# Kernel tuning notes

Hardware: AMD Instinct MI355X
Metric: run time of the kernel (lower is better)

The kernel has to match this reference:

```python
import jax, jax.numpy as jnp
import numpy as np
import math

B, P, M, DPHI, DIN, K, S = 4, 1536, 4, 32, 128, 20, 100


def _gelu(x):
    # BERT tanh-approx GELU, as in the source GELU module
    return 0.5 * x * (1.0 + jnp.tanh(math.sqrt(2.0 / math.pi) * (x + 0.044715 * x ** 3)))


def _softplus(x, beta):
    return jax.nn.softplus(beta * x) / beta


def setup_inputs():
    key = jax.random.key(0)
    ks = jax.random.split(key, 16)
    xav = lambda k, shp: jax.random.normal(k, shp, jnp.float32) * math.sqrt(2.0 / (shp[0] + shp[1]))
    inp = dict(
        values=jax.random.normal(ks[0], (B, P, DPHI), jnp.float32),
        preattention=jax.random.normal(ks[1], (B, P, M), jnp.float32),
        mask=jnp.ones((B, P), jnp.float32),
        seq_times=jnp.sort(jax.random.uniform(ks[2], (B, P), jnp.float32) * 100.0, axis=1),
        taus_u=jax.random.uniform(ks[3], (B, P - 1, 1, S), jnp.float32),
        seq_types=jax.random.randint(ks[4], (B, P), 1, K + 1),
        W_start=xav(ks[5], (DIN, DIN)), b_start=jnp.zeros((DIN,), jnp.float32),
        W_conv=xav(ks[6], (DIN, DIN)), b_conv=jnp.zeros((DIN,), jnp.float32),
        W_dec=xav(ks[7], (DIN, DIN)), b_dec=jnp.zeros((DIN,), jnp.float32),
        W_int=xav(ks[8], (DIN, K)), b_int=jnp.zeros((K,), jnp.float32),
    )
    return inp


def reference(values, preattention, mask, seq_times, taus_u, seq_types,
              W_start, b_start, W_conv, b_conv, W_dec, b_dec, W_int, b_int):
    Bn, Pn, Mn = preattention.shape
    # --- cumulative softmax weighting ---
    A = preattention[:, None, :, :]                                  # [B,1,P,m]
    Cm = jax.lax.cummax(preattention, axis=1)[:, :, None, :]         # [B,P,1,m]
    causal = jnp.triu(jnp.ones((Pn, Pn), bool), 1)[None, :, :, None]  # q > p masked
    D = jnp.exp(jnp.where(causal, -1e30, A - Cm))                    # [B,P,Q,m]
    E = D.sum(2)                                                     # [B,P,m]
    out5 = jnp.einsum('bpqm,bqd->bpmd', D, values) / E[..., None]
    out5 = out5 * mask[:, :, None, None]                             # [B,P,m,d_phi]
    embed = out5.reshape(Bn, Pn, -1)                                 # [B,P,d_in]
    # --- CIF_sahp (mod='mc') ---
    npm = mask
    dt = (seq_times[:, 1:] - seq_times[:, :-1]) * npm[:, 1:]         # [B,T]
    start = _gelu(embed @ W_start + b_start)[:, :-1] * npm[:, 1:, None]
    conv = _gelu(embed @ W_conv + b_conv)[:, :-1] * npm[:, 1:, None]
    omega = _softplus(embed @ W_dec + b_dec, 10.0)[:, :-1] * npm[:, 1:, None]
    cell_t = jnp.tanh(conv + (start - conv) * jnp.exp(-omega * dt[:, :, None]))
    intens = _softplus(cell_t @ W_int + b_int, 1.0)                  # [B,T,K]
    onehot = jax.nn.one_hot(seq_types, K + 1, dtype=jnp.float32)[:, :, 1:]
    sumK = (intens * onehot[:, 1:]).sum(-1)
    sumK = jnp.where(npm[:, 1:] > 0, sumK, 1.0)
    log_sum = jnp.log(sumK).sum(-1)                                  # [B]
    # Monte-Carlo integral of the intensity
    taus = dt[:, :, None, None] * taus_u                             # [B,T,1,S]
    cell_tau = jnp.tanh(conv[:, :, :, None] + (start - conv)[:, :, :, None]
                        * jnp.exp(-omega[:, :, :, None] * taus))     # [B,T,d,S]
    intens_s = _softplus(jnp.einsum('btds,dk->btks', cell_tau, W_int)
                         + b_int[None, None, :, None], 1.0)          # [B,T,K,S]
    intens_s = intens_s * npm[:, 1:, None, None]
    partial = dt * intens_s.sum(2).mean(2)                           # [B,T]
    integral = partial.sum(1)                                        # [B]
    return jnp.stack([log_sum, integral], axis=-1)                   # [B,2]
```

## Files before the change

kernel.cpp:

```cpp
#include <hip/hip_runtime.h>
#include <hip/hip_bf16.h>
#include <math.h>

#define Bv 4
#define Pv 1536
#define Mv 4
#define DPHIv 32
#define DINv 128
#define Kv 20
#define Sv 100
#define TT 4
#define NTB ((Pv - 1 + TT - 1) / TT)
#define ACH 256
#define NCH (Pv / ACH)

typedef short bf16x8 __attribute__((ext_vector_type(8)));
typedef float f32x4 __attribute__((ext_vector_type(4)));

__device__ __forceinline__ float fast_tanh(float x) {
  float e = __expf(2.0f * x);
  return 1.0f - __fdividef(2.0f, e + 1.0f);
}
__device__ __forceinline__ float gelu_f(float x) {
  const float c = 0.7978845608028654f;
  float t = fast_tanh(c * (x + 0.044715f * x * x * x));
  return 0.5f * x * (1.0f + t);
}
__device__ __forceinline__ float softplus1(float y) {
  return fmaxf(y, 0.0f) + log1pf(__expf(-fabsf(y)));
}
__device__ __forceinline__ float softplus10(float x) {
  float y = 10.0f * x;
  return (fmaxf(y, 0.0f) + log1pf(__expf(-fabsf(y)))) * 0.1f;
}

__device__ __forceinline__ int swz(int row, int d) {
  return row * 128 + ((((d >> 3) ^ row) & 7) << 3) + ((d >> 6) << 6) + (d & 7);
}

__global__ __launch_bounds__(256) void attn_kernel(
    const float* __restrict__ values,
    const float* __restrict__ pre,
    const float* __restrict__ mask,
    float* __restrict__ emb)
{
  const int c = blockIdx.x % NCH;
  const int bm = blockIdx.x / NCH;
  const int b = bm >> 2;
  const int m = bm & 3;
  const int tid = threadIdx.x;
  const int end = (c + 1) * ACH;
  const int hb = c * ACH;

  __shared__ float s_e[Pv];
  __shared__ float s_v[ACH * DPHIv];
  __shared__ float s_mk[ACH];
  __shared__ float s_H[8][DPHIv];
  __shared__ float s_HE[8];
  __shared__ float s_mx[4];

  float mx = -1e30f;
  for (int p = tid; p < end; p += 256) mx = fmaxf(mx, pre[(b * Pv + p) * Mv + m]);
#pragma unroll
  for (int o = 32; o > 0; o >>= 1) mx = fmaxf(mx, __shfl_xor(mx, o));
  if ((tid & 63) == 0) s_mx[tid >> 6] = mx;
  __syncthreads();
  mx = fmaxf(fmaxf(s_mx[0], s_mx[1]), fmaxf(s_mx[2], s_mx[3]));

  for (int p = tid; p < end; p += 256)
    s_e[p] = __expf(pre[(b * Pv + p) * Mv + m] - mx);
  for (int i = tid; i < ACH * DPHIv; i += 256)
    s_v[i] = values[(b * Pv + hb) * DPHIv + i];
  if (tid < ACH) s_mk[tid] = mask[b * Pv + hb + tid];
  __syncthreads();

  {
    const int g = tid >> 5, d = tid & 31;
    const int per = hb >> 3;
    float acc = 0.f, accE = 0.f;
    for (int p = g * per; p < (g + 1) * per; ++p) {
      float e = s_e[p];
      accE += e;
      acc = fmaf(e, values[(b * Pv + p) * DPHIv + d], acc);
    }
    s_H[g][d] = acc;
    if (d == 0) s_HE[g] = accE;
  }
  __syncthreads();

  if (tid < DPHIv) {
    float a = 0.f, aE = 0.f;
#pragma unroll
    for (int g = 0; g < 8; ++g) { a += s_H[g][tid]; aE += s_HE[g]; }
    for (int q = 0; q < ACH; ++q) {
      float e = s_e[hb + q];
      aE += e;
      a = fmaf(e, s_v[q * DPHIv + tid], a);
      emb[(b * Pv + hb + q) * DINv + m * DPHIv + tid] =
          __fdividef(a, aE) * s_mk[q];
    }
  }
}

__global__ __launch_bounds__(256, 2) void main_kernel(
    const float* __restrict__ emb,
    const float* __restrict__ mask,
    const float* __restrict__ times,
    const float* __restrict__ taus_u,
    const int* __restrict__ types,
    const float* __restrict__ W_start, const float* __restrict__ b_start,
    const float* __restrict__ W_conv,  const float* __restrict__ b_conv,
    const float* __restrict__ W_dec,   const float* __restrict__ b_dec,
    const float* __restrict__ W_int,   const float* __restrict__ b_int,
    float* __restrict__ out)
{
  const int tid = threadIdx.x;
  const int b = blockIdx.x / NTB;
  const int t0 = (blockIdx.x % NTB) * TT;
  const int lane = tid & 63;
  const int wv = tid >> 6;

  __shared__ float s_emb[TT][DINv];
  __shared__ float s_start[TT][DINv];
  __shared__ float s_conv[TT][DINv];
  __shared__ float s_omega[TT][DINv];
  __shared__ float s_tau[TT][Sv];
  __shared__ __align__(16) short s_cthi[Sv * DINv];
  __shared__ __align__(16) short s_ctlo[Sv * DINv];
  __shared__ __align__(16) short s_wthi[32 * DINv];
  __shared__ __align__(16) short s_wtlo[32 * DINv];
  __shared__ float s_dt[TT], s_npm[TT];
  __shared__ int   s_kt[TT];
  __shared__ float s_bint[Kv];
  __shared__ float s_red[8];

  for (int i = tid; i < 32 * DINv; i += 256) {
    int k = i >> 7, d = i & 127;
    float w = (k < Kv) ? W_int[d * Kv + k] : 0.f;
    __hip_bfloat16 h = __float2bfloat16(w);
    float hf = __bfloat162float(h);
    __hip_bfloat16 l = __float2bfloat16(w - hf);
    int a = swz(k, d);
    s_wthi[a] = *(short*)&h;
    s_wtlo[a] = *(short*)&l;
  }
  if (tid < Kv) s_bint[tid] = b_int[tid];

  for (int i = tid; i < TT * DINv; i += 256) {
    int r = i >> 7, d = i & 127;
    int t = t0 + r;
    s_emb[r][d] = (t < Pv - 1) ? emb[(b * Pv + t) * DINv + d] : 0.f;
  }
  for (int i = tid; i < TT * Sv; i += 256) {
    int r = i / Sv, s = i % Sv;
    int t = t0 + r;
    s_tau[r][s] = (t < Pv - 1) ? taus_u[(b * (Pv - 1) + t) * Sv + s] : 0.f;
  }
  if (tid < TT) {
    int t = t0 + tid;
    float np = 0.f, dtv = 0.f; int kt = 0;
    if (t < Pv - 1) {
      np = mask[b * Pv + t + 1];
      dtv = (times[b * Pv + t + 1] - times[b * Pv + t]) * np;
      int ty = types[b * Pv + t + 1] - 1;
      kt = min(max(ty, 0), Kv - 1);
    }
    s_npm[tid] = np; s_dt[tid] = dtv; s_kt[tid] = kt;
  }
  __syncthreads();

  {
    const int j = tid & 127;
    const int half = tid >> 7;
    for (int round = 0; round < 2; ++round) {
      int which = round * 2 + half;
      if (which < 3) {
        const float* W = (which == 0) ? W_start : (which == 1) ? W_conv : W_dec;
        const float* bias = (which == 0) ? b_start : (which == 1) ? b_conv : b_dec;
        float acc[TT];
#pragma unroll
        for (int r = 0; r < TT; ++r) acc[r] = 0.f;
        for (int d = 0; d < DINv; ++d) {
          float w = W[d * DINv + j];
#pragma unroll
          for (int r = 0; r < TT; ++r) acc[r] = fmaf(s_emb[r][d], w, acc[r]);
        }
        float bj = bias[j];
#pragma unroll
        for (int r = 0; r < TT; ++r) {
          float v = acc[r] + bj;
          float np = s_npm[r];
          if (which == 0)      s_start[r][j] = gelu_f(v) * np;
          else if (which == 1) s_conv[r][j]  = gelu_f(v) * np;
          else                 s_omega[r][j] = softplus10(v) * np;
        }
      }
    }
  }
  __syncthreads();

  float logsum_local = 0.f, integ_local = 0.f;
  const int nr = min(TT, (Pv - 1) - t0);

  const int nt = wv & 1;
  const int mt0 = wv >> 1;
  const int colk = nt * 16 + (lane & 15);
  const float bk = (colk < Kv) ? s_bint[colk] : 0.f;

  for (int r = 0; r < nr; ++r) {
    const float dtv = s_dt[r];

    float pl = 0.f;
    if (tid < DINv) {
      float cv = s_conv[r][tid];
      float dl = s_start[r][tid] - cv;
      float om = s_omega[r][tid];
      float ct = fast_tanh(fmaf(dl, __expf(-om * dtv), cv));
      pl = ct * W_int[tid * Kv + s_kt[r]];
    }

    {
      const int d = tid & 127;
      const int sh = tid >> 7;
      float cv = s_conv[r][d];
      float dl = s_start[r][d] - cv;
      float om = s_omega[r][d];
      float a1 = -om * dtv;
#pragma unroll 2
      for (int ii = 0; ii < Sv / 2; ++ii) {
        int s = 2 * ii + sh;
        float ex = __expf(a1 * s_tau[r][s]);
        float x = fmaf(dl, ex, cv);
        float e2 = __expf(2.0f * x);
        float ct = 1.0f - __fdividef(2.0f, e2 + 1.0f);
        __hip_bfloat16 h = __float2bfloat16(ct);
        float hf = __bfloat162float(h);
        __hip_bfloat16 lo = __float2bfloat16(ct - hf);
        int a = swz(s, d);
        s_cthi[a] = *(short*)&h;
        s_ctlo[a] = *(short*)&lo;
      }
    }
    __syncthreads();

    float psum = 0.f;
    {
      f32x4 a0 = {0.f,0.f,0.f,0.f}, a1 = {0.f,0.f,0.f,0.f};
      f32x4 a2 = {0.f,0.f,0.f,0.f}, a3 = {0.f,0.f,0.f,0.f};
#pragma unroll
      for (int ks = 0; ks < 4; ++ks) {
        const int ub = (ks * 4 + (lane >> 4)) << 3;
        const int baddr = colk * 128 + ((((ub >> 3) ^ colk) & 7) << 3) + ((ub >> 6) << 6);
        bf16x8 bh = *(const bf16x8*)&s_wthi[baddr];
        bf16x8 bl = *(const bf16x8*)&s_wtlo[baddr];
#pragma unroll
        for (int u = 0; u < 4; ++u) {
          int mt = mt0 + 2 * u;
          if (mt < 7) {
            int sr = min(mt * 16 + (lane & 15), Sv - 1);
            int aaddr = sr * 128 + ((((ub >> 3) ^ sr) & 7) << 3) + ((ub >> 6) << 6);
            bf16x8 ah = *(const bf16x8*)&s_cthi[aaddr];
            bf16x8 al = *(const bf16x8*)&s_ctlo[aaddr];
            f32x4 acc = (u == 0) ? a0 : (u == 1) ? a1 : (u == 2) ? a2 : a3;
            acc = __builtin_amdgcn_mfma_f32_16x16x32_bf16(ah, bh, acc, 0, 0, 0);
            acc = __builtin_amdgcn_mfma_f32_16x16x32_bf16(al, bh, acc, 0, 0, 0);
            acc = __builtin_amdgcn_mfma_f32_16x16x32_bf16(ah, bl, acc, 0, 0, 0);
            if (u == 0) a0 = acc; else if (u == 1) a1 = acc; else if (u == 2) a2 = acc; else a3 = acc;
          }
        }
      }
      if (colk < Kv) {
#pragma unroll
        for (int u = 0; u < 4; ++u) {
          int mt = mt0 + 2 * u;
          if (mt < 7) {
            f32x4 acc = (u == 0) ? a0 : (u == 1) ? a1 : (u == 2) ? a2 : a3;
#pragma unroll
            for (int j = 0; j < 4; ++j) {
              int s = mt * 16 + ((lane >> 4) << 2) + j;
              if (s < Sv) psum += softplus1(acc[j] + bk);
            }
          }
        }
      }
    }

    float v0 = pl, v1 = psum;
#pragma unroll
    for (int o = 32; o > 0; o >>= 1) {
      v0 += __shfl_xor(v0, o);
      v1 += __shfl_xor(v1, o);
    }
    if ((tid & 63) == 0) { s_red[wv * 2] = v0; s_red[wv * 2 + 1] = v1; }
    __syncthreads();
    if (tid == 0) {
      float dot = 0.f, tot = 0.f;
#pragma unroll
      for (int w = 0; w < 4; ++w) { dot += s_red[w * 2]; tot += s_red[w * 2 + 1]; }
      float sk = softplus1(dot + s_bint[s_kt[r]]);
      if (s_npm[r] > 0.f) logsum_local += logf(sk);
      integ_local += dtv * tot * (1.0f / Sv);
    }
    __syncthreads();
  }

  if (tid == 0) {
    atomicAdd(&out[b * 2 + 0], logsum_local);
    atomicAdd(&out[b * 2 + 1], integ_local);
  }
}

extern "C" void kernel_launch(void* const* d_in, const int* in_sizes, int n_in,
                              void* d_out, int out_size, void* d_ws, size_t ws_size,
                              hipStream_t stream) {
  const float* values  = (const float*)d_in[0];
  const float* pre     = (const float*)d_in[1];
  const float* mask    = (const float*)d_in[2];
  const float* times   = (const float*)d_in[3];
  const float* tausu   = (const float*)d_in[4];
  const int*   types   = (const int*)d_in[5];
  const float* W_start = (const float*)d_in[6];
  const float* b_start = (const float*)d_in[7];
  const float* W_conv  = (const float*)d_in[8];
  const float* b_conv  = (const float*)d_in[9];
  const float* W_dec   = (const float*)d_in[10];
  const float* b_dec   = (const float*)d_in[11];
  const float* W_int   = (const float*)d_in[12];
  const float* b_int   = (const float*)d_in[13];
  float* out = (float*)d_out;
  float* emb = (float*)d_ws;

  (void)hipMemsetAsync(out, 0, out_size * sizeof(float), stream);
  attn_kernel<<<dim3(Bv * Mv * NCH), dim3(256), 0, stream>>>(values, pre, mask, emb);
  main_kernel<<<dim3(Bv * NTB), dim3(256), 0, stream>>>(
      emb, mask, times, tausu, types,
      W_start, b_start, W_conv, b_conv, W_dec, b_dec, W_int, b_int, out);
}
```

Before: 322.5 us.

## Build MFMA A-fragments in registers, drop shared cell_tau buffer and per-row syncs

The main kernel no longer writes the cell_tau matrix to shared memory as bf16 hi/lo halves. Each wave now computes its tanh values straight into MFMA A-operand registers and covers both K column tiles, which removes the shared stores and loads and the two barriers per row. The hi/lo bf16 split now uses bit masking (truncation) instead of round-to-nearest conversion. Freeing the shared buffer allows raising launch bounds to 3 blocks per CU, and the attention chunk size is halved. In exchange the exp/tanh work is recomputed per wave, the truncated split may shift numerics slightly, and the smaller chunk changes the attention kernel's parallelism.

After: 284.0 us. -11.9%, faster.

```diff
diff --git a/kernel.cpp b/kernel.cpp
--- a/kernel.cpp
+++ b/kernel.cpp
@@ -11,11 +11,13 @@
 #define Sv 100
 #define TT 4
 #define NTB ((Pv - 1 + TT - 1) / TT)
-#define ACH 256
+#define ACH 128
 #define NCH (Pv / ACH)
 
 typedef short bf16x8 __attribute__((ext_vector_type(8)));
 typedef float f32x4 __attribute__((ext_vector_type(4)));
+typedef unsigned int u32;
+typedef u32 u32x4 __attribute__((ext_vector_type(4)));
 
 __device__ __forceinline__ float fast_tanh(float x) {
   float e = __expf(2.0f * x);
@@ -32,10 +34,6 @@
 __device__ __forceinline__ float softplus10(float x) {
   float y = 10.0f * x;
   return (fmaxf(y, 0.0f) + log1pf(__expf(-fabsf(y)))) * 0.1f;
-}
-
-__device__ __forceinline__ int swz(int row, int d) {
-  return row * 128 + ((((d >> 3) ^ row) & 7) << 3) + ((d >> 6) << 6) + (d & 7);
 }
 
 __global__ __launch_bounds__(256) void attn_kernel(
@@ -102,7 +100,7 @@
   }
 }
 
-__global__ __launch_bounds__(256, 2) void main_kernel(
+__global__ __launch_bounds__(256, 3) void main_kernel(
     const float* __restrict__ emb,
     const float* __restrict__ mask,
     const float* __restrict__ times,
@@ -119,30 +117,32 @@
   const int t0 = (blockIdx.x % NTB) * TT;
   const int lane = tid & 63;
   const int wv = tid >> 6;
-
-  __shared__ float s_emb[TT][DINv];
-  __shared__ float s_start[TT][DINv];
-  __shared__ float s_conv[TT][DINv];
-  __shared__ float s_omega[TT][DINv];
+  const int rowq = lane >> 4;
+  const int l15 = lane & 15;
+
+  __shared__ __align__(16) float s_emb[TT][DINv];
+  __shared__ __align__(16) float s_st[TT][DINv];
+  __shared__ __align__(16) float s_cv[TT][DINv];
+  __shared__ __align__(16) float s_nom[TT][DINv];
   __shared__ float s_tau[TT][Sv];
-  __shared__ __align__(16) short s_cthi[Sv * DINv];
-  __shared__ __align__(16) short s_ctlo[Sv * DINv];
   __shared__ __align__(16) short s_wthi[32 * DINv];
   __shared__ __align__(16) short s_wtlo[32 * DINv];
   __shared__ float s_dt[TT], s_npm[TT];
   __shared__ int   s_kt[TT];
   __shared__ float s_bint[Kv];
-  __shared__ float s_red[8];
+  __shared__ float s_red[4];
+  __shared__ float s_ls;
 
   for (int i = tid; i < 32 * DINv; i += 256) {
     int k = i >> 7, d = i & 127;
     float w = (k < Kv) ? W_int[d * Kv + k] : 0.f;
-    __hip_bfloat16 h = __float2bfloat16(w);
-    float hf = __bfloat162float(h);
-    __hip_bfloat16 l = __float2bfloat16(w - hf);
-    int a = swz(k, d);
-    s_wthi[a] = *(short*)&h;
-    s_wtlo[a] = *(short*)&l;
+    u32 wb = __float_as_uint(w);
+    short hi = (short)(wb >> 16);
+    float hf = __uint_as_float(wb & 0xffff0000u);
+    short lo = (short)(__float_as_uint(w - hf) >> 16);
+    int a = k * 128 + ((((d >> 3) ^ k) & 7) << 3) + ((d >> 6) << 6) + (d & 7);
+    s_wthi[a] = hi;
+    s_wtlo[a] = lo;
   }
   if (tid < Kv) s_bint[tid] = b_int[tid];
 
@@ -169,144 +169,142 @@
   }
   __syncthreads();
 
-  {
-    const int j = tid & 127;
-    const int half = tid >> 7;
-    for (int round = 0; round < 2; ++round) {
-      int which = round * 2 + half;
-      if (which < 3) {
-        const float* W = (which == 0) ? W_start : (which == 1) ? W_conv : W_dec;
-        const float* bias = (which == 0) ? b_start : (which == 1) ? b_conv : b_dec;
-        float acc[TT];
-#pragma unroll
-        for (int r = 0; r < TT; ++r) acc[r] = 0.f;
-        for (int d = 0; d < DINv; ++d) {
-          float w = W[d * DINv + j];
-#pragma unroll
-          for (int r = 0; r < TT; ++r) acc[r] = fmaf(s_emb[r][d], w, acc[r]);
-        }
-        float bj = bias[j];
-#pragma unroll
-        for (int r = 0; r < TT; ++r) {
-          float v = acc[r] + bj;
-          float np = s_npm[r];
-          if (which == 0)      s_start[r][j] = gelu_f(v) * np;
-          else if (which == 1) s_conv[r][j]  = gelu_f(v) * np;
-          else                 s_omega[r][j] = softplus10(v) * np;
-        }
-      }
-    }
-  }
-  __syncthreads();
-
-  float logsum_local = 0.f, integ_local = 0.f;
+  for (int task = tid; task < 3 * DINv; task += 256) {
+    const int which = task >> 7;
+    const int j = task & 127;
+    const float* W = (which == 0) ? W_start : (which == 1) ? W_conv : W_dec;
+    const float* bias = (which == 0) ? b_start : (which == 1) ? b_conv : b_dec;
+    float acc[TT];
+#pragma unroll
+    for (int r = 0; r < TT; ++r) acc[r] = 0.f;
+    for (int d = 0; d < DINv; ++d) {
+      float w = W[d * DINv + j];
+#pragma unroll
+      for (int r = 0; r < TT; ++r) acc[r] = fmaf(s_emb[r][d], w, acc[r]);
+    }
+    float bj = bias[j];
+#pragma unroll
+    for (int r = 0; r < TT; ++r) {
+      float v = acc[r] + bj;
+      float np = s_npm[r];
+      if (which == 0)      s_st[r][j]  = gelu_f(v) * np;
+      else if (which == 1) s_cv[r][j]  = gelu_f(v) * np;
+      else                 s_nom[r][j] = -softplus10(v) * np;
+    }
+  }
+  __syncthreads();
+
+  const float bk0 = s_bint[l15];
+  const bool  k1ok = (l15 < Kv - 16);
+  const float bk1 = k1ok ? s_bint[16 + l15] : 0.f;
+
+  float integ = 0.f;
+  float logsum = 0.f;
   const int nr = min(TT, (Pv - 1) - t0);
-
-  const int nt = wv & 1;
-  const int mt0 = wv >> 1;
-  const int colk = nt * 16 + (lane & 15);
-  const float bk = (colk < Kv) ? s_bint[colk] : 0.f;
+  const int mtA = wv;
+  const int mtB = wv + 4;
+
+#define BUILD_AND_MMA(MT, ACC0, ACC1)                                          \
+  {                                                                            \
+    int sr = (MT) * 16 + l15; if (sr > Sv - 1) sr = Sv - 1;                    \
+    const float p = dtv * s_tau[r][sr];                                        \
+    _Pragma("unroll")                                                          \
+    for (int ks = 0; ks < 4; ++ks) {                                           \
+      const int ub = (ks * 4 + rowq) << 3;                                     \
+      f32x4 cvA = *(const f32x4*)&s_cv[r][ub];                                 \
+      f32x4 cvB = *(const f32x4*)&s_cv[r][ub + 4];                             \
+      f32x4 stA = *(const f32x4*)&s_st[r][ub];                                 \
+      f32x4 stB = *(const f32x4*)&s_st[r][ub + 4];                             \
+      f32x4 nmA = *(const f32x4*)&s_nom[r][ub];                                \
+      f32x4 nmB = *(const f32x4*)&s_nom[r][ub + 4];                            \
+      float ct[8];                                                             \
+      _Pragma("unroll")                                                        \
+      for (int j = 0; j < 4; ++j) {                                            \
+        float e0 = __expf(nmA[j] * p);                                         \
+        float x0 = fmaf(stA[j] - cvA[j], e0, cvA[j]);                          \
+        float q0 = __expf(2.0f * x0);                                          \
+        ct[j] = 1.0f - __fdividef(2.0f, q0 + 1.0f);                            \
+        float e1 = __expf(nmB[j] * p);                                         \
+        float x1 = fmaf(stB[j] - cvB[j], e1, cvB[j]);                          \
+        float q1 = __expf(2.0f * x1);                                          \
+        ct[j + 4] = 1.0f - __fdividef(2.0f, q1 + 1.0f);                        \
+      }                                                                        \
+      u32x4 hv, lv;                                                            \
+      _Pragma("unroll")                                                        \
+      for (int q = 0; q < 4; ++q) {                                            \
+        u32 b0 = __float_as_uint(ct[2 * q]);                                   \
+        u32 b1 = __float_as_uint(ct[2 * q + 1]);                               \
+        hv[q] = (b0 >> 16) | (b1 & 0xffff0000u);                               \
+        float f0 = ct[2 * q]     - __uint_as_float(b0 & 0xffff0000u);          \
+        float f1 = ct[2 * q + 1] - __uint_as_float(b1 & 0xffff0000u);          \
+        lv[q] = (__float_as_uint(f0) >> 16) | (__float_as_uint(f1) & 0xffff0000u); \
+      }                                                                        \
+      bf16x8 ah = __builtin_bit_cast(bf16x8, hv);                              \
+      bf16x8 al = __builtin_bit_cast(bf16x8, lv);                              \
+      const int ba0 = l15 * 128 + ((((ub >> 3) ^ l15) & 7) << 3) + ((ub >> 6) << 6); \
+      bf16x8 bh0 = *(const bf16x8*)&s_wthi[ba0];                               \
+      bf16x8 bl0 = *(const bf16x8*)&s_wtlo[ba0];                               \
+      bf16x8 bh1 = *(const bf16x8*)&s_wthi[ba0 + 2048];                        \
+      bf16x8 bl1 = *(const bf16x8*)&s_wtlo[ba0 + 2048];                        \
+      ACC0 = __builtin_amdgcn_mfma_f32_16x16x32_bf16(ah, bh0, ACC0, 0, 0, 0);  \
+      ACC0 = __builtin_amdgcn_mfma_f32_16x16x32_bf16(al, bh0, ACC0, 0, 0, 0);  \
+      ACC0 = __builtin_amdgcn_mfma_f32_16x16x32_bf16(ah, bl0, ACC0, 0, 0, 0);  \
+      ACC1 = __builtin_amdgcn_mfma_f32_16x16x32_bf16(ah, bh1, ACC1, 0, 0, 0);  \
+      ACC1 = __builtin_amdgcn_mfma_f32_16x16x32_bf16(al, bh1, ACC1, 0, 0, 0);  \
+      ACC1 = __builtin_amdgcn_mfma_f32_16x16x32_bf16(ah, bl1, ACC1, 0, 0, 0);  \
+    }                                                                          \
+  }
+
+#define EPILOGUE(MT, ACC0, ACC1)                                               \
+  {                                                                            \
+    float ps = 0.f;                                                            \
+    _Pragma("unroll")                                                          \
+    for (int jj = 0; jj < 4; ++jj) {                                           \
+      int s = (MT) * 16 + rowq * 4 + jj;                                       \
+      if (s < Sv) {                                                            \
+        ps += softplus1(ACC0[jj] + bk0);                                       \
+        if (k1ok) ps += softplus1(ACC1[jj] + bk1);                             \
+      }                                                                        \
+    }                                                                          \
+    integ += dtv * ps;                                                         \
+  }
 
   for (int r = 0; r < nr; ++r) {
     const float dtv = s_dt[r];
 
-    float pl = 0.f;
-    if (tid < DINv) {
-      float cv = s_conv[r][tid];
-      float dl = s_start[r][tid] - cv;
-      float om = s_omega[r][tid];
-      float ct = fast_tanh(fmaf(dl, __expf(-om * dtv), cv));
-      pl = ct * W_int[tid * Kv + s_kt[r]];
-    }
-
-    {
-      const int d = tid & 127;
-      const int sh = tid >> 7;
-      float cv = s_conv[r][d];
-      float dl = s_start[r][d] - cv;
-      float om = s_omega[r][d];
-      float a1 = -om * dtv;
-#pragma unroll 2
-      for (int ii = 0; ii < Sv / 2; ++ii) {
-        int s = 2 * ii + sh;
-        float ex = __expf(a1 * s_tau[r][s]);
-        float x = fmaf(dl, ex, cv);
-        float e2 = __expf(2.0f * x);
-        float ct = 1.0f - __fdividef(2.0f, e2 + 1.0f);
-        __hip_bfloat16 h = __float2bfloat16(ct);
-        float hf = __bfloat162float(h);
-        __hip_bfloat16 lo = __float2bfloat16(ct - hf);
-        int a = swz(s, d);
-        s_cthi[a] = *(short*)&h;
-        s_ctlo[a] = *(short*)&lo;
+    if (wv == 3) {
+      float pl = 0.f;
+#pragma unroll
+      for (int h = 0; h < 2; ++h) {
+        int d = lane + 64 * h;
+        float cv = s_cv[r][d];
+        float e = __expf(s_nom[r][d] * dtv);
+        float x = fmaf(s_st[r][d] - cv, e, cv);
+        pl = fmaf(fast_tanh(x), W_int[d * Kv + s_kt[r]], pl);
       }
-    }
-    __syncthreads();
-
-    float psum = 0.f;
-    {
-      f32x4 a0 = {0.f,0.f,0.f,0.f}, a1 = {0.f,0.f,0.f,0.f};
-      f32x4 a2 = {0.f,0.f,0.f,0.f}, a3 = {0.f,0.f,0.f,0.f};
-#pragma unroll
-      for (int ks = 0; ks < 4; ++ks) {
-        const int ub = (ks * 4 + (lane >> 4)) << 3;
-        const int baddr = colk * 128 + ((((ub >> 3) ^ colk) & 7) << 3) + ((ub >> 6) << 6);
-        bf16x8 bh = *(const bf16x8*)&s_wthi[baddr];
-        bf16x8 bl = *(const bf16x8*)&s_wtlo[baddr];
-#pragma unroll
-        for (int u = 0; u < 4; ++u) {
-          int mt = mt0 + 2 * u;
-          if (mt < 7) {
-            int sr = min(mt * 16 + (lane & 15), Sv - 1);
-            int aaddr = sr * 128 + ((((ub >> 3) ^ sr) & 7) << 3) + ((ub >> 6) << 6);
-            bf16x8 ah = *(const bf16x8*)&s_cthi[aaddr];
-            bf16x8 al = *(const bf16x8*)&s_ctlo[aaddr];
-            f32x4 acc = (u == 0) ? a0 : (u == 1) ? a1 : (u == 2) ? a2 : a3;
-            acc = __builtin_amdgcn_mfma_f32_16x16x32_bf16(ah, bh, acc, 0, 0, 0);
-            acc = __builtin_amdgcn_mfma_f32_16x16x32_bf16(al, bh, acc, 0, 0, 0);
-            acc = __builtin_amdgcn_mfma_f32_16x16x32_bf16(ah, bl, acc, 0, 0, 0);
-            if (u == 0) a0 = acc; else if (u == 1) a1 = acc; else if (u == 2) a2 = acc; else a3 = acc;
-          }
-        }
-      }
-      if (colk < Kv) {
-#pragma unroll
-        for (int u = 0; u < 4; ++u) {
-          int mt = mt0 + 2 * u;
-          if (mt < 7) {
-            f32x4 acc = (u == 0) ? a0 : (u == 1) ? a1 : (u == 2) ? a2 : a3;
-#pragma unroll
-            for (int j = 0; j < 4; ++j) {
-              int s = mt * 16 + ((lane >> 4) << 2) + j;
-              if (s < Sv) psum += softplus1(acc[j] + bk);
-            }
-          }
-        }
-      }
-    }
-
-    float v0 = pl, v1 = psum;
-#pragma unroll
-    for (int o = 32; o > 0; o >>= 1) {
-      v0 += __shfl_xor(v0, o);
-      v1 += __shfl_xor(v1, o);
-    }
-    if ((tid & 63) == 0) { s_red[wv * 2] = v0; s_red[wv * 2 + 1] = v1; }
-    __syncthreads();
-    if (tid == 0) {
-      float dot = 0.f, tot = 0.f;
-#pragma unroll
-      for (int w = 0; w < 4; ++w) { dot += s_red[w * 2]; tot += s_red[w * 2 + 1]; }
-      float sk = softplus1(dot + s_bint[s_kt[r]]);
-      if (s_npm[r] > 0.f) logsum_local += logf(sk);
-      integ_local += dtv * tot * (1.0f / Sv);
-    }
-    __syncthreads();
-  }
-
+#pragma unroll
+      for (int o = 32; o > 0; o >>= 1) pl += __shfl_xor(pl, o);
+      if (lane == 0 && s_npm[r] > 0.f)
+        logsum += logf(softplus1(pl + s_bint[s_kt[r]]));
+    }
+
+    f32x4 z = {0.f, 0.f, 0.f, 0.f};
+    f32x4 aA0 = z, aA1 = z, aB0 = z, aB1 = z;
+    BUILD_AND_MMA(mtA, aA0, aA1);
+    if (mtB < 7) BUILD_AND_MMA(mtB, aB0, aB1);
+    EPILOGUE(mtA, aA0, aA1);
+    if (mtB < 7) EPILOGUE(mtB, aB0, aB1);
+  }
+
+#pragma unroll
+  for (int o = 32; o > 0; o >>= 1) integ += __shfl_xor(integ, o);
+  if (lane == 0) s_red[wv] = integ;
+  if (wv == 3 && lane == 0) s_ls = logsum;
+  __syncthreads();
   if (tid == 0) {
-    atomicAdd(&out[b * 2 + 0], logsum_local);
-    atomicAdd(&out[b * 2 + 1], integ_local);
+    atomicAdd(&out[b * 2 + 0], s_ls);
+    atomicAdd(&out[b * 2 + 1],
+              (s_red[0] + s_red[1] + s_red[2] + s_red[3]) * (1.0f / Sv));
   }
 }
 
```
